# Optimization experiments

Hardware: AMD Instinct MI355X
Metric: run time of the kernel (lower is better)

## Reference

```python
import jax, jax.numpy as jnp
import numpy as np

B, S, D = 2, 4096, 768
H = 12
HD = D // H  # 64


def setup_inputs() -> dict:
    key = jax.random.key(0)
    ks = jax.random.split(key, 5)
    scale = 1.0 / np.sqrt(D)
    x = jax.random.normal(ks[0], (B, S, D), dtype=jnp.float32)
    Wq = jax.random.normal(ks[1], (D, D), dtype=jnp.float32) * scale
    Wk = jax.random.normal(ks[2], (D, D), dtype=jnp.float32) * scale
    Wv = jax.random.normal(ks[3], (D, D), dtype=jnp.float32) * scale
    Wo = jax.random.normal(ks[4], (D, D), dtype=jnp.float32) * scale
    zb = jnp.zeros((D,), dtype=jnp.float32)
    return {"x": x, "Wq": Wq, "bq": zb, "Wk": Wk, "bk": zb, "Wv": Wv, "bv": zb, "Wo": Wo, "bo": zb}


def reference(x, Wq, bq, Wk, bk, Wv, bv, Wo, bo):
    b, s, d = x.shape
    # projections: nn.Linear computes x @ W^T + b; here W is stored as [in, out]-style [D, D]
    def proj(W, bias):
        y = jnp.einsum('bsd,ed->bse', x, W) + bias  # matches torch Linear (weight [out,in])
        return y.reshape(b, s, H, HD).transpose(0, 2, 1, 3)  # [B,H,S,HD]
    q = proj(Wq, bq)
    k = proj(Wk, bk)
    v = proj(Wv, bv)
    att = jnp.einsum('bhqd,bhkd->bhqk', q, k) / np.sqrt(HD).astype(np.float32)
    causal = jnp.tril(jnp.ones((s, s), dtype=bool))
    att = jnp.where(causal, att, -jnp.inf)
    att = jax.nn.softmax(att, axis=-1)  # dropout p=0 (eval)
    y = jnp.einsum('bhqk,bhkd->bhqd', att, v)
    y = y.transpose(0, 2, 1, 3).reshape(b, s, d)
    return jnp.einsum('bsd,ed->bse', y, Wo) + bo
```

## Files before the change

kernel.cpp:

```cpp
#include <hip/hip_runtime.h>
#include <hip/hip_bf16.h>

typedef __bf16 bf16;
typedef __attribute__((ext_vector_type(8))) __bf16 bf16x8;
typedef __attribute__((ext_vector_type(4))) __bf16 bf16x4;
typedef __attribute__((ext_vector_type(4))) float f32x4;
typedef __attribute__((ext_vector_type(16))) float f32x16;

#if __has_builtin(__builtin_amdgcn_permlane32_swap)
#define HAVE_PLSWAP 1
typedef __attribute__((ext_vector_type(2))) unsigned uint2v;
#endif

#define MFMA16(a, b, c) __builtin_amdgcn_mfma_f32_16x16x32_bf16((a), (b), (c), 0, 0, 0)
#define MFMA32(a, b, c) __builtin_amdgcn_mfma_f32_32x32x16_bf16((a), (b), (c), 0, 0, 0)

__device__ __forceinline__ void gload_lds16(const bf16* g, bf16* l) {
  __builtin_amdgcn_global_load_lds(
      (const __attribute__((address_space(1))) void*)g,
      (__attribute__((address_space(3))) void*)l, 16, 0, 0);
}

__device__ __forceinline__ unsigned pkbf(float a, float b) {
  union { unsigned u; bf16 h[2]; } w;
  w.h[0] = (bf16)a; w.h[1] = (bf16)b;
  return w.u;
}

#define CBAR(N)                                               \
  do {                                                        \
    asm volatile("s_waitcnt vmcnt(" #N ") lgkmcnt(0)" ::: "memory"); \
    __builtin_amdgcn_s_barrier();                             \
    __builtin_amdgcn_sched_barrier(0);                        \
  } while (0)

__global__ void cvt_all(const float* __restrict__ x,
                        const float* __restrict__ wq, const float* __restrict__ wk,
                        const float* __restrict__ wv, const float* __restrict__ wo,
                        bf16* __restrict__ xb, bf16* __restrict__ Wb) {
  constexpr int NX4 = 6291456 / 4;
  constexpr int NW4 = 589824 / 4;
  constexpr int TOT = NX4 + 4 * NW4;
  int stride = gridDim.x * blockDim.x;
  for (int i = blockIdx.x * blockDim.x + threadIdx.x; i < TOT; i += stride) {
    const float4* src;
    bf16x4* dst;
    if (i < NX4) {
      src = reinterpret_cast<const float4*>(x) + i;
      dst = reinterpret_cast<bf16x4*>(xb) + i;
    } else {
      int j = i - NX4;
      int w = j / NW4, r = j - w * NW4;
      const float* sp = (w == 0) ? wq : (w == 1) ? wk : (w == 2) ? wv : wo;
      src = reinterpret_cast<const float4*>(sp) + r;
      dst = reinterpret_cast<bf16x4*>(Wb) + j;
    }
    float4 v = *src;
    bf16x4 o = {(bf16)v.x, (bf16)v.y, (bf16)v.z, (bf16)v.w};
    *dst = o;
  }
}

template <bool OUT_BF16>
__global__ __launch_bounds__(256) void gemm_bt(
    const bf16* __restrict__ A, const bf16* __restrict__ W,
    const float* __restrict__ b0, const float* __restrict__ b1, const float* __restrict__ b2,
    float* __restrict__ Cf, bf16* __restrict__ Cb,
    int M, int N, int K) {
  const int z = blockIdx.z;
  const bf16* Wz = W + (size_t)z * N * K;
  const float* bias = (z == 0) ? b0 : (z == 1 ? b1 : b2);

  __shared__ alignas(16) bf16 As[128 * 64];
  __shared__ alignas(16) bf16 Bs[128 * 64];

  const int tid = threadIdx.x;
  const int wave = tid >> 6, lane = tid & 63;
  const int lr = lane & 15, lg = lane >> 4;
  const int wr = wave >> 1, wc = wave & 1;
  const int m0 = blockIdx.y * 128, n0 = blockIdx.x * 128;

  f32x4 acc[4][4] = {};

  for (int k0 = 0; k0 < K; k0 += 64) {
    __syncthreads();
#pragma unroll
    for (int j = 0; j < 4; ++j) {
      int cb = j * 256 + wave * 64;
      int c = cb + lane;
      int row = c >> 3, x = c & 7;
      int xs = x ^ (row & 7);
      gload_lds16(&A[(size_t)(m0 + row) * K + k0 + xs * 8], &As[cb * 8]);
      gload_lds16(&Wz[(size_t)(n0 + row) * K + k0 + xs * 8], &Bs[cb * 8]);
    }
    __syncthreads();
#pragma unroll
    for (int kk = 0; kk < 2; ++kk) {
      bf16x8 af[4], bfr[4];
#pragma unroll
      for (int m = 0; m < 4; ++m) {
        int row = wr * 64 + m * 16 + lr;
        int ch = (kk * 4 + lg) ^ (row & 7);
        af[m] = *reinterpret_cast<const bf16x8*>(&As[row * 64 + ch * 8]);
      }
#pragma unroll
      for (int n = 0; n < 4; ++n) {
        int row = wc * 64 + n * 16 + lr;
        int ch = (kk * 4 + lg) ^ (row & 7);
        bfr[n] = *reinterpret_cast<const bf16x8*>(&Bs[row * 64 + ch * 8]);
      }
      __builtin_amdgcn_s_setprio(1);
#pragma unroll
      for (int m = 0; m < 4; ++m)
#pragma unroll
        for (int n = 0; n < 4; ++n)
          acc[m][n] = MFMA16(af[m], bfr[n], acc[m][n]);
      __builtin_amdgcn_s_setprio(0);
    }
  }

#pragma unroll
  for (int m = 0; m < 4; ++m) {
#pragma unroll
    for (int n = 0; n < 4; ++n) {
#pragma unroll
      for (int i = 0; i < 4; ++i) {
        int row = m0 + wr * 64 + m * 16 + lg * 4 + i;
        int col = n0 + wc * 64 + n * 16 + lr;
        float v = acc[m][n][i] + bias[col];
        if constexpr (OUT_BF16)
          (Cb + (size_t)z * M * N)[(size_t)row * N + col] = (bf16)v;
        else
          Cf[(size_t)row * N + col] = v;
      }
    }
  }
}

__global__ __launch_bounds__(256, 3) void attn32(
    const bf16* __restrict__ Q, const bf16* __restrict__ K,
    const bf16* __restrict__ V, bf16* __restrict__ Y) {
  constexpr int S = 4096, D = 768;
  const int lin = blockIdx.x;
  const int xcd = lin & 7, idx = lin >> 3;
  const int seg = idx >> 5;
  const int pair = xcd * 3 + seg;
  const int jj = idx & 31;
  const int f = (seg == 0) ? jj
              : (seg == 1) ? ((jj + 16) & 31)
              : (jj < 16 ? 30 - 2 * jj : 63 - 2 * jj);
  const int h = pair % 12, bb = pair / 12;

  const int tid = threadIdx.x, wave = tid >> 6, lane = tid & 63;
  const int ln = lane & 31, hi = lane >> 5;

  const int qs = (wave < 2) ? (63 - f) : f;
  const int qw0 = qs * 64 + (wave & 1) * 32;
  const int qrow = qw0 + ln;
  const int nt = 64 - f;

  __shared__ alignas(16) bf16 Ks[3][64 * 64];
  __shared__ alignas(16) bf16 Vt[2][64 * 64];

  const size_t head = (size_t)bb * S * D + (size_t)h * 64;
  const float SC2 = 0.125f * 1.44269504089f;

  union U32x4 { unsigned u[4]; bf16x8 v; };
  U32x4 onesU;
  onesU.u[0] = onesU.u[1] = onesU.u[2] = onesU.u[3] = 0x3F803F80u;
  const bf16x8 onesf = onesU.v;

  const f32x16 z16 = {};

  bf16x8 qf[4];
  {
    const bf16* qp = Q + head + (size_t)qrow * D;
#pragma unroll
    for (int c = 0; c < 4; ++c) {
      bf16x8 tq = *reinterpret_cast<const bf16x8*>(qp + c * 16 + hi * 8);
#pragma unroll
      for (int e = 0; e < 8; ++e) tq[e] = (bf16)((float)tq[e] * SC2);
      qf[c] = tq;
    }
  }

  int fOff[4];
#pragma unroll
  for (int i = 0; i < 4; ++i)
    fOff[i] = ln * 64 + ((((2 * i + hi) ^ ln) & 7) * 8);

  const bf16* gk[2];
  int ldsK[2];
#pragma unroll
  for (int j2 = 0; j2 < 2; ++j2) {
    int c = j2 * 256 + tid;
    int r = c >> 3, ch = c & 7;
    gk[j2] = K + head + (size_t)r * D + ((ch ^ (r & 7)) & 7) * 8;
    ldsK[j2] = (j2 * 256 + wave * 64) * 8;
  }

  const int k0v = (tid & 31) * 2, d0 = (tid >> 5) * 8;
  const bf16* gv0 = V + head + (size_t)k0v * D + d0;
  const bf16* gv1 = gv0 + D;
  int wOff[8];
#pragma unroll
  for (int e = 0; e < 8; ++e)
    wOff[e] = (d0 + e) * 64 + ((((k0v >> 3) ^ e) & 7) * 8) + (k0v & 7);

  f32x16 accO0 = {}, accO1 = {}, accL = {};

  auto stageK = [&](int buf) {
#pragma unroll
    for (int j2 = 0; j2 < 2; ++j2) {
      gload_lds16(gk[j2], &Ks[buf][ldsK[j2]]);
      gk[j2] += 64 * D;
    }
  };
  auto loadV = [&](bf16x8* vv) {
    vv[0] = *reinterpret_cast<const bf16x8*>(gv0);
    vv[1] = *reinterpret_cast<const bf16x8*>(gv1);
    gv0 += 64 * D;
    gv1 += 64 * D;
  };
  auto writeV = [&](const bf16x8* vv, int buf) {
#pragma unroll
    for (int e = 0; e < 8; ++e) {
      union { unsigned u; bf16 h[2]; } pw;
      pw.h[0] = vv[0][e]; pw.h[1] = vv[1][e];
      *reinterpret_cast<unsigned*>(&Vt[buf][wOff[e]]) = pw.u;
    }
  };

  {
    bf16x8 v0[2];
    loadV(v0);
    stageK(0);
    stageK(1);
    writeV(v0, 0);
  }
  CBAR(2);

  int curV = 0, curK = 0, sK = 2;
  for (int t = 0; t < nt; ++t) {
    const int kv0 = t * 64;
    const bool more = (t + 1 < nt);
    bf16x8 vnext[2];
    if (more) {
      loadV(vnext);
      if (t + 2 < nt) { stageK(sK); sK = (sK == 2) ? 0 : sK + 1; }
    }

    if (kv0 <= qw0 + 31) {
      const bf16* ksp = &Ks[curK][0];
      f32x16 s0, s1;
      __builtin_amdgcn_s_setprio(1);
      {
        bf16x8 kf0 = *reinterpret_cast<const bf16x8*>(ksp + fOff[0]);
        bf16x8 kf1 = *reinterpret_cast<const bf16x8*>(ksp + fOff[0] + 2048);
        s0 = MFMA32(kf0, qf[0], z16);
        s1 = MFMA32(kf1, qf[0], z16);
      }
#pragma unroll
      for (int c = 1; c < 4; ++c) {
        bf16x8 kf0 = *reinterpret_cast<const bf16x8*>(ksp + fOff[c]);
        bf16x8 kf1 = *reinterpret_cast<const bf16x8*>(ksp + fOff[c] + 2048);
        s0 = MFMA32(kf0, qf[c], s0);
        s1 = MFMA32(kf1, qf[c], s1);
      }
      __builtin_amdgcn_s_setprio(0);

      if (kv0 + 63 > qw0) {
#pragma unroll
        for (int r = 0; r < 16; ++r) {
          int kl = (r & 3) + 8 * (r >> 2) + 4 * hi;
          if (kv0 + kl > qrow) s0[r] = -1e30f;
          if (kv0 + 32 + kl > qrow) s1[r] = -1e30f;
        }
      }

      float p[32];
#pragma unroll
      for (int r = 0; r < 16; ++r) {
        p[r] = __builtin_amdgcn_exp2f(s0[r]);
        p[16 + r] = __builtin_amdgcn_exp2f(s1[r]);
      }

      const bf16* vtp = &Vt[curV][0];
      __builtin_amdgcn_s_setprio(1);
#pragma unroll
      for (int kg = 0; kg < 2; ++kg) {
        const float* pv = &p[kg * 16];
        unsigned w0 = pkbf(pv[0], pv[1]), w1 = pkbf(pv[2], pv[3]);
        unsigned w2 = pkbf(pv[4], pv[5]), w3 = pkbf(pv[6], pv[7]);
        unsigned w4 = pkbf(pv[8], pv[9]), w5 = pkbf(pv[10], pv[11]);
        unsigned w6 = pkbf(pv[12], pv[13]), w7 = pkbf(pv[14], pv[15]);
        union { unsigned u[4]; bf16x8 v; } fe, fo;
#if HAVE_PLSWAP
        uint2v r02 = __builtin_amdgcn_permlane32_swap(w0, w2, false, false);
        uint2v r13 = __builtin_amdgcn_permlane32_swap(w1, w3, false, false);
        uint2v r46 = __builtin_amdgcn_permlane32_swap(w4, w6, false, false);
        uint2v r57 = __builtin_amdgcn_permlane32_swap(w5, w7, false, false);
        fe.u[0] = r02.x; fe.u[1] = r13.x; fe.u[2] = r02.y; fe.u[3] = r13.y;
        fo.u[0] = r46.x; fo.u[1] = r57.x; fo.u[2] = r46.y; fo.u[3] = r57.y;
#else
        unsigned X0 = hi ? w0 : w2, X1 = hi ? w1 : w3;
        unsigned X2 = hi ? w4 : w6, X3 = hi ? w5 : w7;
        unsigned Y0 = __shfl_xor((int)X0, 32), Y1 = __shfl_xor((int)X1, 32);
        unsigned Y2 = __shfl_xor((int)X2, 32), Y3 = __shfl_xor((int)X3, 32);
        fe.u[0] = hi ? Y0 : w0; fe.u[1] = hi ? Y1 : w1;
        fe.u[2] = hi ? w2 : Y0; fe.u[3] = hi ? w3 : Y1;
        fo.u[0] = hi ? Y2 : w4; fo.u[1] = hi ? Y3 : w5;
        fo.u[2] = hi ? w6 : Y2; fo.u[3] = hi ? w7 : Y3;
#endif
#pragma unroll
        for (int half = 0; half < 2; ++half) {
          int kc = 2 * kg + half;
          bf16x8 pf = half ? fo.v : fe.v;
          bf16x8 vf0 = *reinterpret_cast<const bf16x8*>(vtp + fOff[kc]);
          bf16x8 vf1 = *reinterpret_cast<const bf16x8*>(vtp + fOff[kc] + 2048);
          accO0 = MFMA32(vf0, pf, accO0);
          accO1 = MFMA32(vf1, pf, accO1);
          accL = MFMA32(onesf, pf, accL);
        }
      }
      __builtin_amdgcn_s_setprio(0);
    }

    if (more) {
      writeV(vnext, curV ^ 1);
      CBAR(2);
      curV ^= 1;
      curK = (curK == 2) ? 0 : curK + 1;
    }
  }

  float inv = 1.f / accL[0];
  bf16* yp = Y + head + (size_t)qrow * D;
#pragma unroll
  for (int g = 0; g < 4; ++g) {
    bf16x4 o0, o1;
#pragma unroll
    for (int i = 0; i < 4; ++i) {
      o0[i] = (bf16)(accO0[g * 4 + i] * inv);
      o1[i] = (bf16)(accO1[g * 4 + i] * inv);
    }
    *reinterpret_cast<bf16x4*>(yp + 8 * g + 4 * hi) = o0;
    *reinterpret_cast<bf16x4*>(yp + 32 + 8 * g + 4 * hi) = o1;
  }
}

extern "C" void kernel_launch(void* const* d_in, const int* in_sizes, int n_in,
                              void* d_out, int out_size, void* d_ws, size_t ws_size,
                              hipStream_t stream) {
  const float* x  = (const float*)d_in[0];
  const float* Wq = (const float*)d_in[1];
  const float* bq = (const float*)d_in[2];
  const float* Wk = (const float*)d_in[3];
  const float* bk = (const float*)d_in[4];
  const float* Wv = (const float*)d_in[5];
  const float* bv = (const float*)d_in[6];
  const float* Wo = (const float*)d_in[7];
  const float* bo = (const float*)d_in[8];
  float* out = (float*)d_out;

  constexpr int Bx = 2, S = 4096, Dd = 768;
  constexpr int M = Bx * S;
  constexpr size_t XB = (size_t)M * Dd;
  constexpr size_t WB = (size_t)Dd * Dd;

  char* ws = (char*)d_ws;
  bf16* xb = (bf16*)ws;
  bf16* Wb = (bf16*)(ws + 2 * XB);
  bf16* Qb = (bf16*)(ws + 2 * XB + 8 * WB);
  bf16* Kb = Qb + XB;
  bf16* Vb = Kb + XB;
  bf16* Yb = Vb + XB;

  cvt_all<<<2048, 256, 0, stream>>>(x, Wq, Wk, Wv, Wo, xb, Wb);

  gemm_bt<true><<<dim3(6, 64, 3), 256, 0, stream>>>(
      xb, Wb, bq, bk, bv, nullptr, Qb, M, Dd, Dd);

  attn32<<<dim3(768), 256, 0, stream>>>(Qb, Kb, Vb, Yb);

  gemm_bt<false><<<dim3(6, 64, 1), 256, 0, stream>>>(
      Yb, Wb + 3 * WB, bo, bo, bo, out, nullptr, M, Dd, Dd);
}
```

Before: 183.3 us.

## Software-pipeline QK^T one tile ahead with a four-slot K ring

Restructures the attention loop so the QK^T MFMAs for the next KV tile are issued before the softmax and PV work of the current tile, using ping-pong score registers and a loop unrolled by two. The K staging ring grows from three to four LDS slots so K is prefetched three tiles ahead. The aim is to overlap matrix-core work with the exp and pack work and hide LDS latency. In exchange it holds a second set of score registers and uses more LDS, which may lower occupancy.

Result: slower. 236.6 us (+29.1%).

```diff
diff --git a/kernel.cpp b/kernel.cpp
--- a/kernel.cpp
+++ b/kernel.cpp
@@ -159,7 +159,7 @@
   const int qrow = qw0 + ln;
   const int nt = 64 - f;
 
-  __shared__ alignas(16) bf16 Ks[3][64 * 64];
+  __shared__ alignas(16) bf16 Ks[4][64 * 64];
   __shared__ alignas(16) bf16 Vt[2][64 * 64];
 
   const size_t head = (size_t)bb * S * D + (size_t)h * 64;
@@ -231,107 +231,116 @@
     }
   };
 
+  auto qkInto = [&](f32x16& n0, f32x16& n1, const bf16* ksp) {
+    {
+      bf16x8 kf0 = *reinterpret_cast<const bf16x8*>(ksp + fOff[0]);
+      bf16x8 kf1 = *reinterpret_cast<const bf16x8*>(ksp + fOff[0] + 2048);
+      n0 = MFMA32(kf0, qf[0], z16);
+      n1 = MFMA32(kf1, qf[0], z16);
+    }
+#pragma unroll
+    for (int c = 1; c < 4; ++c) {
+      bf16x8 kf0 = *reinterpret_cast<const bf16x8*>(ksp + fOff[c]);
+      bf16x8 kf1 = *reinterpret_cast<const bf16x8*>(ksp + fOff[c] + 2048);
+      n0 = MFMA32(kf0, qf[c], n0);
+      n1 = MFMA32(kf1, qf[c], n1);
+    }
+  };
+
+  auto consume = [&](int t, f32x16& c0, f32x16& c1) {
+    const int kv0 = t * 64;
+    if (kv0 + 63 > qw0) {
+#pragma unroll
+      for (int r = 0; r < 16; ++r) {
+        int kl = (r & 3) + 8 * (r >> 2) + 4 * hi;
+        if (kv0 + kl > qrow) c0[r] = -1e30f;
+        if (kv0 + 32 + kl > qrow) c1[r] = -1e30f;
+      }
+    }
+    float p[32];
+#pragma unroll
+    for (int r = 0; r < 16; ++r) {
+      p[r] = __builtin_amdgcn_exp2f(c0[r]);
+      p[16 + r] = __builtin_amdgcn_exp2f(c1[r]);
+    }
+    const bf16* vtp = &Vt[t & 1][0];
+    __builtin_amdgcn_s_setprio(1);
+#pragma unroll
+    for (int kg = 0; kg < 2; ++kg) {
+      const float* pv = &p[kg * 16];
+      unsigned w0 = pkbf(pv[0], pv[1]), w1 = pkbf(pv[2], pv[3]);
+      unsigned w2 = pkbf(pv[4], pv[5]), w3 = pkbf(pv[6], pv[7]);
+      unsigned w4 = pkbf(pv[8], pv[9]), w5 = pkbf(pv[10], pv[11]);
+      unsigned w6 = pkbf(pv[12], pv[13]), w7 = pkbf(pv[14], pv[15]);
+      union { unsigned u[4]; bf16x8 v; } fe, fo;
+#if HAVE_PLSWAP
+      uint2v r02 = __builtin_amdgcn_permlane32_swap(w0, w2, false, false);
+      uint2v r13 = __builtin_amdgcn_permlane32_swap(w1, w3, false, false);
+      uint2v r46 = __builtin_amdgcn_permlane32_swap(w4, w6, false, false);
+      uint2v r57 = __builtin_amdgcn_permlane32_swap(w5, w7, false, false);
+      fe.u[0] = r02.x; fe.u[1] = r13.x; fe.u[2] = r02.y; fe.u[3] = r13.y;
+      fo.u[0] = r46.x; fo.u[1] = r57.x; fo.u[2] = r46.y; fo.u[3] = r57.y;
+#else
+      unsigned X0 = hi ? w0 : w2, X1 = hi ? w1 : w3;
+      unsigned X2 = hi ? w4 : w6, X3 = hi ? w5 : w7;
+      unsigned Y0 = __shfl_xor((int)X0, 32), Y1 = __shfl_xor((int)X1, 32);
+      unsigned Y2 = __shfl_xor((int)X2, 32), Y3 = __shfl_xor((int)X3, 32);
+      fe.u[0] = hi ? Y0 : w0; fe.u[1] = hi ? Y1 : w1;
+      fe.u[2] = hi ? w2 : Y0; fe.u[3] = hi ? w3 : Y1;
+      fo.u[0] = hi ? Y2 : w4; fo.u[1] = hi ? Y3 : w5;
+      fo.u[2] = hi ? w6 : Y2; fo.u[3] = hi ? w7 : Y3;
+#endif
+#pragma unroll
+      for (int half = 0; half < 2; ++half) {
+        int kc = 2 * kg + half;
+        bf16x8 pf = half ? fo.v : fe.v;
+        bf16x8 vf0 = *reinterpret_cast<const bf16x8*>(vtp + fOff[kc]);
+        bf16x8 vf1 = *reinterpret_cast<const bf16x8*>(vtp + fOff[kc] + 2048);
+        accO0 = MFMA32(vf0, pf, accO0);
+        accO1 = MFMA32(vf1, pf, accO1);
+        accL = MFMA32(onesf, pf, accL);
+      }
+    }
+    __builtin_amdgcn_s_setprio(0);
+  };
+
+  auto body = [&](int t, f32x16& c0, f32x16& c1, f32x16& n0, f32x16& n1) {
+    const int kv0 = t * 64;
+    const bool more = (t + 1 < nt);
+    bf16x8 vnext[2];
+    if (more) {
+      loadV(vnext);
+      if (t + 3 < nt) stageK((t + 3) & 3);
+    }
+    if (more && (kv0 + 64 <= qw0 + 31))
+      qkInto(n0, n1, &Ks[(t + 1) & 3][0]);
+    if (kv0 <= qw0 + 31)
+      consume(t, c0, c1);
+    if (more) {
+      writeV(vnext, (t + 1) & 1);
+      CBAR(2);
+    }
+  };
+
   {
     bf16x8 v0[2];
     loadV(v0);
     stageK(0);
     stageK(1);
+    stageK(2);
     writeV(v0, 0);
   }
   CBAR(2);
 
-  int curV = 0, curK = 0, sK = 2;
-  for (int t = 0; t < nt; ++t) {
-    const int kv0 = t * 64;
-    const bool more = (t + 1 < nt);
-    bf16x8 vnext[2];
-    if (more) {
-      loadV(vnext);
-      if (t + 2 < nt) { stageK(sK); sK = (sK == 2) ? 0 : sK + 1; }
-    }
-
-    if (kv0 <= qw0 + 31) {
-      const bf16* ksp = &Ks[curK][0];
-      f32x16 s0, s1;
-      __builtin_amdgcn_s_setprio(1);
-      {
-        bf16x8 kf0 = *reinterpret_cast<const bf16x8*>(ksp + fOff[0]);
-        bf16x8 kf1 = *reinterpret_cast<const bf16x8*>(ksp + fOff[0] + 2048);
-        s0 = MFMA32(kf0, qf[0], z16);
-        s1 = MFMA32(kf1, qf[0], z16);
-      }
-#pragma unroll
-      for (int c = 1; c < 4; ++c) {
-        bf16x8 kf0 = *reinterpret_cast<const bf16x8*>(ksp + fOff[c]);
-        bf16x8 kf1 = *reinterpret_cast<const bf16x8*>(ksp + fOff[c] + 2048);
-        s0 = MFMA32(kf0, qf[c], s0);
-        s1 = MFMA32(kf1, qf[c], s1);
-      }
-      __builtin_amdgcn_s_setprio(0);
-
-      if (kv0 + 63 > qw0) {
-#pragma unroll
-        for (int r = 0; r < 16; ++r) {
-          int kl = (r & 3) + 8 * (r >> 2) + 4 * hi;
-          if (kv0 + kl > qrow) s0[r] = -1e30f;
-          if (kv0 + 32 + kl > qrow) s1[r] = -1e30f;
-        }
-      }
-
-      float p[32];
-#pragma unroll
-      for (int r = 0; r < 16; ++r) {
-        p[r] = __builtin_amdgcn_exp2f(s0[r]);
-        p[16 + r] = __builtin_amdgcn_exp2f(s1[r]);
-      }
-
-      const bf16* vtp = &Vt[curV][0];
-      __builtin_amdgcn_s_setprio(1);
-#pragma unroll
-      for (int kg = 0; kg < 2; ++kg) {
-        const float* pv = &p[kg * 16];
-        unsigned w0 = pkbf(pv[0], pv[1]), w1 = pkbf(pv[2], pv[3]);
-        unsigned w2 = pkbf(pv[4], pv[5]), w3 = pkbf(pv[6], pv[7]);
-        unsigned w4 = pkbf(pv[8], pv[9]), w5 = pkbf(pv[10], pv[11]);
-        unsigned w6 = pkbf(pv[12], pv[13]), w7 = pkbf(pv[14], pv[15]);
-        union { unsigned u[4]; bf16x8 v; } fe, fo;
-#if HAVE_PLSWAP
-        uint2v r02 = __builtin_amdgcn_permlane32_swap(w0, w2, false, false);
-        uint2v r13 = __builtin_amdgcn_permlane32_swap(w1, w3, false, false);
-        uint2v r46 = __builtin_amdgcn_permlane32_swap(w4, w6, false, false);
-        uint2v r57 = __builtin_amdgcn_permlane32_swap(w5, w7, false, false);
-        fe.u[0] = r02.x; fe.u[1] = r13.x; fe.u[2] = r02.y; fe.u[3] = r13.y;
-        fo.u[0] = r46.x; fo.u[1] = r57.x; fo.u[2] = r46.y; fo.u[3] = r57.y;
-#else
-        unsigned X0 = hi ? w0 : w2, X1 = hi ? w1 : w3;
-        unsigned X2 = hi ? w4 : w6, X3 = hi ? w5 : w7;
-        unsigned Y0 = __shfl_xor((int)X0, 32), Y1 = __shfl_xor((int)X1, 32);
-        unsigned Y2 = __shfl_xor((int)X2, 32), Y3 = __shfl_xor((int)X3, 32);
-        fe.u[0] = hi ? Y0 : w0; fe.u[1] = hi ? Y1 : w1;
-        fe.u[2] = hi ? w2 : Y0; fe.u[3] = hi ? w3 : Y1;
-        fo.u[0] = hi ? Y2 : w4; fo.u[1] = hi ? Y3 : w5;
-        fo.u[2] = hi ? w6 : Y2; fo.u[3] = hi ? w7 : Y3;
-#endif
-#pragma unroll
-        for (int half = 0; half < 2; ++half) {
-          int kc = 2 * kg + half;
-          bf16x8 pf = half ? fo.v : fe.v;
-          bf16x8 vf0 = *reinterpret_cast<const bf16x8*>(vtp + fOff[kc]);
-          bf16x8 vf1 = *reinterpret_cast<const bf16x8*>(vtp + fOff[kc] + 2048);
-          accO0 = MFMA32(vf0, pf, accO0);
-          accO1 = MFMA32(vf1, pf, accO1);
-          accL = MFMA32(onesf, pf, accL);
-        }
-      }
-      __builtin_amdgcn_s_setprio(0);
-    }
-
-    if (more) {
-      writeV(vnext, curV ^ 1);
-      CBAR(2);
-      curV ^= 1;
-      curK = (curK == 2) ? 0 : curK + 1;
-    }
+  f32x16 sA0, sA1, sB0, sB1;
+  qkInto(sA0, sA1, &Ks[0][0]);
+
+  int t = 0;
+  while (true) {
+    body(t, sA0, sA1, sB0, sB1);
+    if (++t >= nt) break;
+    body(t, sB0, sB1, sA0, sA1);
+    if (++t >= nt) break;
   }
 
   float inv = 1.f / accL[0];
```
